# Kernel tuning notes

Measured on AMD Instinct MI355X. Metric: run time of the kernel, lower is better.

## Reference

```python
import jax, jax.numpy as jnp
import numpy as np

EPS = 1e-5  # eqx.nn.LayerNorm default


def _layer_norm(x, w, b):
    m = x.mean(-1, keepdims=True)
    v = ((x - m) ** 2).mean(-1, keepdims=True)
    return (x - m) / jnp.sqrt(v + EPS) * w + b


def _s4_block(x, nw, nb, lre, lim, bre, bim, cre, cim, d, lstep, ow, ob, o2w, o2b):
    # x: [L, H]. One SequenceBlock: LayerNorm -> S4 recurrence (lax.scan) -> GELU -> GLU-style gated linear -> residual.
    skip = x
    h = _layer_norm(x, nw, nb)
    Lam = lre + 1j * lim                      # [H, N] complex diagonal state matrix
    step = jnp.exp(lstep)[:, None]            # [H, 1] per-channel timescale
    BL = 1.0 / (1.0 - (step / 2.0) * Lam)     # bilinear discretization
    Abar = BL * (1.0 + (step / 2.0) * Lam)    # [H, N]
    Bbar = BL * step * (bre + 1j * bim)       # [H, N]
    C = cre + 1j * cim                        # [H, N]

    def scan_fn(state, u):                    # state: [H, N] complex, u: [H]
        new = Abar * state + Bbar * u[:, None]
        y = 2.0 * jnp.sum(C * new, axis=-1).real + d * u
        return new, y

    init = jnp.zeros(Abar.shape, Abar.dtype)  # cell.init_state
    _, y = jax.lax.scan(scan_fn, init, h)     # [L, H]
    y = jax.nn.gelu(y)
    y = (y @ ow.T + ob) * jax.nn.sigmoid(y @ o2w.T + o2b)
    return skip + y


def setup_inputs() -> dict:
    key = jax.random.key(0)
    L, IN, OUT, H, N, NL = 2048, 4, 3, 512, 32, 4
    ks = jax.random.split(key, 16)
    return {
        "x": jax.random.normal(ks[0], (L, IN), jnp.float32),
        "enc_w": jax.random.normal(ks[1], (H, IN), jnp.float32) / np.sqrt(IN),
        "enc_b": jnp.zeros((H,), jnp.float32),
        "dec_w": jax.random.normal(ks[2], (OUT, H), jnp.float32) / np.sqrt(H),
        "dec_b": jnp.zeros((OUT,), jnp.float32),
        "norm_w": jnp.ones((NL, H), jnp.float32),
        "norm_b": jnp.zeros((NL, H), jnp.float32),
        "lam_re": -0.5 - jax.random.uniform(ks[3], (NL, H, N), jnp.float32),  # stable (Re < 0)
        "lam_im": np.pi * jax.random.normal(ks[4], (NL, H, N), jnp.float32),
        "b_re": jax.random.normal(ks[5], (NL, H, N), jnp.float32) / np.sqrt(N),
        "b_im": jax.random.normal(ks[6], (NL, H, N), jnp.float32) / np.sqrt(N),
        "c_re": jax.random.normal(ks[7], (NL, H, N), jnp.float32) / np.sqrt(N),
        "c_im": jax.random.normal(ks[8], (NL, H, N), jnp.float32) / np.sqrt(N),
        "d": jax.random.normal(ks[9], (NL, H), jnp.float32),
        "log_step": float(np.log(1e-3)) + float(np.log(1e-1) - np.log(1e-3)) * jax.random.uniform(ks[10], (NL, H), jnp.float32),
        "out_w": jax.random.normal(ks[11], (NL, H, H), jnp.float32) / np.sqrt(H),
        "out_b": jnp.zeros((NL, H), jnp.float32),
        "out2_w": jax.random.normal(ks[12], (NL, H, H), jnp.float32) / np.sqrt(H),
        "out2_b": jnp.zeros((NL, H), jnp.float32),
    }


def reference(x, enc_w, enc_b, dec_w, dec_b, norm_w, norm_b, lam_re, lam_im, b_re, b_im, c_re, c_im, d, log_step, out_w, out_b, out2_w, out2_b):
    h = x @ enc_w.T + enc_b                   # encoder: [L, IN] -> [L, H]
    for i in range(norm_w.shape[0]):          # fixed small n_layers loop
        h = _s4_block(h, norm_w[i], norm_b[i], lam_re[i], lam_im[i], b_re[i], b_im[i],
                      c_re[i], c_im[i], d[i], log_step[i], out_w[i], out_b[i], out2_w[i], out2_b[i])
    return h @ dec_w.T + dec_b                # decoder: [L, H] -> [L, OUT]
```

## Files before the change

kernel.cpp:

```cpp
#include <hip/hip_runtime.h>
#include <hip/hip_bf16.h>
#include <math.h>

#define LSEQ 2048
#define HD   512
#define NST  32
#define LC   32
#define NCHK 64
#define SUP  8
#define NSUP 8
#define HH   (HD * HD)

typedef __bf16 bf16;
typedef __bf16 bf16x8 __attribute__((ext_vector_type(8)));
typedef float  floatx4 __attribute__((ext_vector_type(4)));

__device__ __forceinline__ float wave_reduce_add(float v) {
#pragma unroll
    for (int m = 32; m; m >>= 1) v += __shfl_xor(v, m, 64);
    return v;
}

__device__ __forceinline__ float gelu_tanh(float x) {
    float z = 0.7978845608028654f * (x + 0.044715f * x * x * x);
    float e = __expf(2.f * z);
    float th = 1.f - 2.f / (e + 1.f);
    return 0.5f * x * (1.f + th);
}

__device__ __forceinline__ void make_ab(float lre, float lim, float step,
                                        float br0, float bi0,
                                        float& ar, float& ai, float& br, float& bi) {
    float s2 = 0.5f * step;
    float dr = 1.f - s2 * lre, di = -s2 * lim;
    float inv = 1.f / (dr * dr + di * di);
    float blr = dr * inv, bli = -di * inv;
    float nr = 1.f + s2 * lre, ni = s2 * lim;
    ar = blr * nr - bli * ni;
    ai = blr * ni + bli * nr;
    float tr = step * br0, ti = step * bi0;
    br = blr * tr - bli * ti;
    bi = blr * ti + bli * tr;
}

__global__ __launch_bounds__(256) void prep_kernel(
    const float* __restrict__ lre, const float* __restrict__ lim,
    const float* __restrict__ bre, const float* __restrict__ bim,
    const float* __restrict__ cre, const float* __restrict__ cim,
    const float* __restrict__ ls,
    float2* __restrict__ cA, float2* __restrict__ cB,
    float2* __restrict__ cC, float2* __restrict__ cAp) {
    int tid = blockIdx.x * 256 + threadIdx.x;
    int lay = tid >> 14, rem = tid & 16383;
    int ch = rem >> 5, n = rem & 31;
    int src = tid;
    float step = __expf(ls[lay * HD + ch]);
    float ar, ai, br, bi;
    make_ab(lre[src], lim[src], step, bre[src], bim[src], ar, ai, br, bi);
    float xr = ar, xi = ai;
#pragma unroll
    for (int q = 0; q < 5; ++q) { float tt = xr * xr - xi * xi; xi = 2.f * xr * xi; xr = tt; }
    int dst = (lay * NST + n) * HD + ch;
    cA[dst]  = make_float2(ar, ai);
    cB[dst]  = make_float2(br, bi);
    cC[dst]  = make_float2(2.f * cre[src], 2.f * cim[src]);
    cAp[dst] = make_float2(xr, xi);
}

__global__ __launch_bounds__(256) void cvt_kernel(
    const float* __restrict__ ow, const float* __restrict__ o2w,
    bf16* __restrict__ wb) {
    const float* src = blockIdx.y ? o2w : ow;
    bf16* dst = wb + blockIdx.y * (4 * HH);
    int i = (blockIdx.x * 256 + threadIdx.x) * 8;
    float4 a = *(const float4*)(src + i);
    float4 b = *(const float4*)(src + i + 4);
    bf16x8 o;
    o[0] = (bf16)a.x; o[1] = (bf16)a.y; o[2] = (bf16)a.z; o[3] = (bf16)a.w;
    o[4] = (bf16)b.x; o[5] = (bf16)b.y; o[6] = (bf16)b.z; o[7] = (bf16)b.w;
    *(bf16x8*)(dst + i) = o;
}

__global__ __launch_bounds__(256) void enc_kernel(
    const float* __restrict__ x, const float* __restrict__ w,
    const float* __restrict__ b, float* __restrict__ h) {
    int idx = blockIdx.x * 256 + threadIdx.x;
    int t = idx >> 9, i = idx & (HD - 1);
    float acc = b[i];
    float4 xv = *(const float4*)(x + t * 4);
    float4 wv = *(const float4*)(w + i * 4);
    acc = fmaf(xv.x, wv.x, acc);
    acc = fmaf(xv.y, wv.y, acc);
    acc = fmaf(xv.z, wv.z, acc);
    acc = fmaf(xv.w, wv.w, acc);
    h[idx] = acc;
}

__global__ __launch_bounds__(256) void ln_kernel(
    const float* __restrict__ h, float* __restrict__ hn,
    const float* __restrict__ w, const float* __restrict__ b) {
    int wv = threadIdx.x >> 6, lane = threadIdx.x & 63;
    int row = blockIdx.x * 4 + wv;
    const float* hp = h + row * HD + lane * 8;
    float v[8];
    *(float4*)(v)     = *(const float4*)(hp);
    *(float4*)(v + 4) = *(const float4*)(hp + 4);
    float s = 0.f;
#pragma unroll
    for (int e = 0; e < 8; ++e) s += v[e];
    s = wave_reduce_add(s);
    float m = s * (1.f / HD);
    float q = 0.f;
#pragma unroll
    for (int e = 0; e < 8; ++e) { float d = v[e] - m; q += d * d; }
    q = wave_reduce_add(q);
    float rstd = rsqrtf(q * (1.f / HD) + 1e-5f);
    float w8[8], b8[8];
    *(float4*)(w8)     = *(const float4*)(w + lane * 8);
    *(float4*)(w8 + 4) = *(const float4*)(w + lane * 8 + 4);
    *(float4*)(b8)     = *(const float4*)(b + lane * 8);
    *(float4*)(b8 + 4) = *(const float4*)(b + lane * 8 + 4);
    float o[8];
#pragma unroll
    for (int e = 0; e < 8; ++e)
        o[e] = (v[e] - m) * rstd * w8[e] + b8[e];
    float* op = hn + row * HD + lane * 8;
    *(float4*)op       = *(float4*)o;
    *(float4*)(op + 4) = *(float4*)(o + 4);
}

__global__ __launch_bounds__(256, 2) void p1_kernel(
    const float* __restrict__ u,
    const float2* __restrict__ cA, const float2* __restrict__ cB,
    float2* __restrict__ f, int lay) {
    __shared__ float tile[4 * LC * 16];
    int tid = threadIdx.x;
    int lane = tid & 63, w = tid >> 6;
    int chl = lane & 15;
    int ch = blockIdx.x * 16 + chl;
    int sub = lane >> 4;
    int chunk = blockIdx.y * 4 + w;
    int t0 = blockIdx.y * 4 * LC;
    const float* ub = u + (size_t)t0 * HD + blockIdx.x * 16;
#pragma unroll
    for (int r = 0; r < 8; ++r) {
        int idx = r * 256 + tid;
        tile[idx] = ub[(idx >> 4) * HD + (idx & 15)];
    }
    int cbase = (lay * NST + sub * 8) * HD + ch;
    float aR[8], aI[8], bR[8], bI[8];
#pragma unroll
    for (int j = 0; j < 8; ++j) {
        float2 t = cA[cbase + j * HD]; aR[j] = t.x; aI[j] = t.y;
        t = cB[cbase + j * HD];        bR[j] = t.x; bI[j] = t.y;
    }
    float sr[8], si[8];
#pragma unroll
    for (int j = 0; j < 8; ++j) { sr[j] = 0.f; si[j] = 0.f; }
    __syncthreads();
    const float* tp = tile + (w * LC) * 16 + chl;
#pragma unroll 4
    for (int t = 0; t < LC; ++t) {
        float uu = tp[t * 16];
#pragma unroll
        for (int j = 0; j < 8; ++j) {
            float nr = fmaf(aR[j], sr[j], fmaf(-aI[j], si[j], bR[j] * uu));
            float ni = fmaf(aI[j], sr[j], fmaf( aR[j], si[j], bI[j] * uu));
            sr[j] = nr; si[j] = ni;
        }
    }
    float2* fp = f + (chunk * NST + sub * 8) * HD + ch;
#pragma unroll
    for (int j = 0; j < 8; ++j) fp[j * HD] = make_float2(sr[j], si[j]);
}

__global__ __launch_bounds__(256) void p2a_kernel(
    float2* __restrict__ f, const float2* __restrict__ cAp, int lay) {
    int tg = blockIdx.x * 256 + threadIdx.x;
    int ch = tg & 511;
    int ns = tg >> 9;
    int n = ns & 31, sup = ns >> 5;
    float2 ap = cAp[(lay * NST + n) * HD + ch];
    float2* fp = f + ((sup * SUP) * NST + n) * HD + ch;
    float sr = 0.f, si = 0.f;
#pragma unroll
    for (int j = 0; j < SUP; ++j) {
        float2 v = fp[(size_t)j * NST * HD];
        float nr = fmaf(ap.x, sr, fmaf(-ap.y, si, v.x));
        float ni = fmaf(ap.y, sr, fmaf( ap.x, si, v.y));
        sr = nr; si = ni;
        fp[(size_t)j * NST * HD] = make_float2(sr, si);
    }
}

__global__ __launch_bounds__(256) void p2b_kernel(
    float2* __restrict__ f, const float2* __restrict__ cAp, int lay) {
    int tg = blockIdx.x * 256 + threadIdx.x;
    int ch = tg & 511, n = tg >> 9;
    float2 ap = cAp[(lay * NST + n) * HD + ch];
    float xr = ap.x, xi = ap.y;
#pragma unroll
    for (int q = 0; q < 3; ++q) { float tt = xr * xr - xi * xi; xi = 2.f * xr * xi; xr = tt; }
    float2* fp = f + ((SUP - 1) * NST + n) * HD + ch;
    const size_t stride = (size_t)SUP * NST * HD;
    float sr = 0.f, si = 0.f;
#pragma unroll
    for (int k = 0; k < NSUP; ++k) {
        float2 v = fp[k * stride];
        float nr = fmaf(xr, sr, fmaf(-xi, si, v.x));
        float ni = fmaf(xi, sr, fmaf( xr, si, v.y));
        sr = nr; si = ni;
        fp[k * stride] = make_float2(sr, si);
    }
}

__global__ __launch_bounds__(256) void p2c_kernel(
    float2* __restrict__ f, const float2* __restrict__ cAp, int lay) {
    int tg = blockIdx.x * 256 + threadIdx.x;
    int ch = tg & 511;
    int ns = tg >> 9;
    int n = ns & 31, sup = ns >> 5;
    if (sup == 0) return;
    float2 ap = cAp[(lay * NST + n) * HD + ch];
    float2 S = f[((sup * SUP - 1) * NST + n) * HD + ch];
    float2* fp = f + ((sup * SUP) * NST + n) * HD + ch;
    float wr = ap.x, wi = ap.y;
#pragma unroll
    for (int j = 0; j < SUP - 1; ++j) {
        float2 v = fp[(size_t)j * NST * HD];
        v.x += wr * S.x - wi * S.y;
        v.y += wr * S.y + wi * S.x;
        fp[(size_t)j * NST * HD] = v;
        float nwr = wr * ap.x - wi * ap.y;
        float nwi = wr * ap.y + wi * ap.x;
        wr = nwr; wi = nwi;
    }
}

__global__ __launch_bounds__(256, 2) void p3_kernel(
    const float* __restrict__ u, const float2* __restrict__ f,
    const float2* __restrict__ cA, const float2* __restrict__ cB,
    const float2* __restrict__ cC, const float* __restrict__ d_p,
    bf16* __restrict__ g, int lay) {
    __shared__ float tile[4 * LC * 16];
    int tid = threadIdx.x;
    int lane = tid & 63, w = tid >> 6;
    int chl = lane & 15;
    int ch = blockIdx.x * 16 + chl;
    int sub = lane >> 4;
    int chunk = blockIdx.y * 4 + w;
    int t0 = blockIdx.y * 4 * LC;
    const float* ub = u + (size_t)t0 * HD + blockIdx.x * 16;
#pragma unroll
    for (int r = 0; r < 8; ++r) {
        int idx = r * 256 + tid;
        tile[idx] = ub[(idx >> 4) * HD + (idx & 15)];
    }
    int cbase = (lay * NST + sub * 8) * HD + ch;
    float aR[8], aI[8], bR[8], bI[8], cR[8], cI[8];
#pragma unroll
    for (int j = 0; j < 8; ++j) {
        float2 t = cA[cbase + j * HD]; aR[j] = t.x; aI[j] = t.y;
        t = cB[cbase + j * HD];        bR[j] = t.x; bI[j] = t.y;
        t = cC[cbase + j * HD];        cR[j] = t.x; cI[j] = t.y;
    }
    float dch = d_p[lay * HD + ch];
    float sr[8], si[8];
    if (chunk > 0) {
        const float2* ip = f + ((chunk - 1) * NST + sub * 8) * HD + ch;
#pragma unroll
        for (int j = 0; j < 8; ++j) { float2 v = ip[j * HD]; sr[j] = v.x; si[j] = v.y; }
    } else {
#pragma unroll
        for (int j = 0; j < 8; ++j) { sr[j] = 0.f; si[j] = 0.f; }
    }
    __syncthreads();
    const float* tp = tile + (w * LC) * 16 + chl;
    bf16* gp = g + (size_t)chunk * LC * HD + ch;
#pragma unroll 4
    for (int t = 0; t < LC; ++t) {
        float uu = tp[t * 16];
        float p = 0.f;
#pragma unroll
        for (int j = 0; j < 8; ++j) {
            float nr = fmaf(aR[j], sr[j], fmaf(-aI[j], si[j], bR[j] * uu));
            float ni = fmaf(aI[j], sr[j], fmaf( aR[j], si[j], bI[j] * uu));
            sr[j] = nr; si[j] = ni;
            p = fmaf(cR[j], nr, fmaf(-cI[j], ni, p));
        }
        p += __shfl_xor(p, 16);
        p += __shfl_xor(p, 32);
        float y = fmaf(dch, uu, p);
        if (sub == 0) gp[t * HD] = (bf16)gelu_tanh(y);
    }
}

__global__ __launch_bounds__(256) void mm_kernel(
    const bf16* __restrict__ A,
    const bf16* __restrict__ W1,
    const bf16* __restrict__ W2,
    const float* __restrict__ bias1, const float* __restrict__ bias2,
    float* __restrict__ Hio) {
    const int w = threadIdx.x >> 6, lane = threadIdx.x & 63;
    const int wm = w >> 1, wn = w & 1;
    const int mBase = blockIdx.y * 64 + wm * 32;
    const int nBase = blockIdx.x * 64 + wn * 32;
    const int lrow = lane & 15, quad = lane >> 4;

    floatx4 acc1[2][2] = {{{0.f,0.f,0.f,0.f},{0.f,0.f,0.f,0.f}},{{0.f,0.f,0.f,0.f},{0.f,0.f,0.f,0.f}}};
    floatx4 acc2[2][2] = {{{0.f,0.f,0.f,0.f},{0.f,0.f,0.f,0.f}},{{0.f,0.f,0.f,0.f},{0.f,0.f,0.f,0.f}}};

    for (int k0 = 0; k0 < HD; k0 += 32) {
        int kk = k0 + quad * 8;
        bf16x8 a0 = *(const bf16x8*)(A + (mBase + lrow) * HD + kk);
        bf16x8 a1 = *(const bf16x8*)(A + (mBase + 16 + lrow) * HD + kk);
        bf16x8 p0 = *(const bf16x8*)(W1 + (nBase + lrow) * HD + kk);
        bf16x8 p1 = *(const bf16x8*)(W1 + (nBase + 16 + lrow) * HD + kk);
        bf16x8 q0 = *(const bf16x8*)(W2 + (nBase + lrow) * HD + kk);
        bf16x8 q1 = *(const bf16x8*)(W2 + (nBase + 16 + lrow) * HD + kk);
        acc1[0][0] = __builtin_amdgcn_mfma_f32_16x16x32_bf16(a0, p0, acc1[0][0], 0, 0, 0);
        acc1[0][1] = __builtin_amdgcn_mfma_f32_16x16x32_bf16(a0, p1, acc1[0][1], 0, 0, 0);
        acc1[1][0] = __builtin_amdgcn_mfma_f32_16x16x32_bf16(a1, p0, acc1[1][0], 0, 0, 0);
        acc1[1][1] = __builtin_amdgcn_mfma_f32_16x16x32_bf16(a1, p1, acc1[1][1], 0, 0, 0);
        acc2[0][0] = __builtin_amdgcn_mfma_f32_16x16x32_bf16(a0, q0, acc2[0][0], 0, 0, 0);
        acc2[0][1] = __builtin_amdgcn_mfma_f32_16x16x32_bf16(a0, q1, acc2[0][1], 0, 0, 0);
        acc2[1][0] = __builtin_amdgcn_mfma_f32_16x16x32_bf16(a1, q0, acc2[1][0], 0, 0, 0);
        acc2[1][1] = __builtin_amdgcn_mfma_f32_16x16x32_bf16(a1, q1, acc2[1][1], 0, 0, 0);
    }

#pragma unroll
    for (int fm = 0; fm < 2; ++fm)
#pragma unroll
        for (int fn = 0; fn < 2; ++fn) {
            int j = nBase + fn * 16 + lrow;
            float bb1 = bias1[j], bb2 = bias2[j];
#pragma unroll
            for (int r = 0; r < 4; ++r) {
                int t = mBase + fm * 16 + quad * 4 + r;
                float z1 = acc1[fm][fn][r] + bb1;
                float z2 = acc2[fm][fn][r] + bb2;
                float val = z1 / (1.f + __expf(-z2));
                Hio[t * HD + j] += val;
            }
        }
}

__global__ __launch_bounds__(192) void dec_kernel(
    const float* __restrict__ h, const float* __restrict__ w,
    const float* __restrict__ b, float* __restrict__ out) {
    int j = threadIdx.x >> 6, lane = threadIdx.x & 63;
    int t = blockIdx.x;
    const float* hp = h + t * HD + lane * 8;
    float v[8];
    *(float4*)(v)     = *(const float4*)(hp);
    *(float4*)(v + 4) = *(const float4*)(hp + 4);
    float w8[8];
    *(float4*)(w8)     = *(const float4*)(w + j * HD + lane * 8);
    *(float4*)(w8 + 4) = *(const float4*)(w + j * HD + lane * 8 + 4);
    float s = 0.f;
#pragma unroll
    for (int e = 0; e < 8; ++e) s = fmaf(v[e], w8[e], s);
    s = wave_reduce_add(s);
    if (lane == 0) out[t * 3 + j] = s + b[j];
}

extern "C" void kernel_launch(void* const* d_in, const int* in_sizes, int n_in,
                              void* d_out, int out_size, void* d_ws, size_t ws_size,
                              hipStream_t stream) {
    const float* x   = (const float*)d_in[0];
    const float* ew  = (const float*)d_in[1];
    const float* eb  = (const float*)d_in[2];
    const float* dw  = (const float*)d_in[3];
    const float* db  = (const float*)d_in[4];
    const float* nw  = (const float*)d_in[5];
    const float* nb  = (const float*)d_in[6];
    const float* lre = (const float*)d_in[7];
    const float* lim = (const float*)d_in[8];
    const float* bre = (const float*)d_in[9];
    const float* bim = (const float*)d_in[10];
    const float* cre = (const float*)d_in[11];
    const float* cim = (const float*)d_in[12];
    const float* dd  = (const float*)d_in[13];
    const float* ls  = (const float*)d_in[14];
    const float* ow  = (const float*)d_in[15];
    const float* ob  = (const float*)d_in[16];
    const float* o2w = (const float*)d_in[17];
    const float* o2b = (const float*)d_in[18];

    char* ws = (char*)d_ws;
    float*  h   = (float*)ws;
    float*  hn  = (float*)(ws + (4  << 20));
    float2* f   = (float2*)(ws + (8  << 20));
    bf16*   g   = (bf16*)(ws + (24 << 20));
    bf16*   wb  = (bf16*)(ws + (26 << 20));
    float2* cA  = (float2*)(ws + (30 << 20));
    float2* cB  = (float2*)(ws + (30 << 20) + (512 << 10));
    float2* cC  = (float2*)(ws + (31 << 20));
    float2* cAp = (float2*)(ws + (31 << 20) + (512 << 10));

    prep_kernel<<<256, 256, 0, stream>>>(lre, lim, bre, bim, cre, cim, ls, cA, cB, cC, cAp);
    cvt_kernel<<<dim3(4 * HH / (256 * 8), 2), 256, 0, stream>>>(ow, o2w, wb);
    enc_kernel<<<LSEQ * HD / 256, 256, 0, stream>>>(x, ew, eb, h);
    for (int lay = 0; lay < 4; ++lay) {
        int oH = lay * HD;
        ln_kernel<<<LSEQ / 4, 256, 0, stream>>>(h, hn, nw + oH, nb + oH);
        p1_kernel<<<dim3(HD / 16, NCHK / 4), 256, 0, stream>>>(hn, cA, cB, f, lay);
        p2a_kernel<<<512, 256, 0, stream>>>(f, cAp, lay);
        p2b_kernel<<<64, 256, 0, stream>>>(f, cAp, lay);
        p2c_kernel<<<512, 256, 0, stream>>>(f, cAp, lay);
        p3_kernel<<<dim3(HD / 16, NCHK / 4), 256, 0, stream>>>(hn, f, cA, cB, cC, dd, g, lay);
        mm_kernel<<<dim3(HD / 64, LSEQ / 64), 256, 0, stream>>>(
            g, wb + lay * HH, wb + 4 * HH + lay * HH, ob + oH, o2b + oH, h);
    }
    dec_kernel<<<LSEQ, 192, 0, stream>>>(h, dw, db, (float*)d_out);
}
```

Before: 315.2 us.

## Fuse all stages into one persistent cooperative kernel with grid syncs

Replaces the 31-launch pipeline (prep, convert, encoder, per-layer LN, scan phases, GEMM, decoder) with a single cooperative kernel of 256 blocks that separates stages with grid.sync. LayerNorm is reduced to per-row stats and applied on the fly inside the scan phases, so the normalized activations are no longer written and read back. The intra-chunk scan reads activations through a shared-memory tile. A fallback keeps the old multi-kernel path if the cooperative launch fails. The aim is to remove launch overhead and inter-kernel gaps. The cost is that every phase is fixed at 256 blocks of 256 threads, which may lower occupancy for the GEMM and scan phases, and each grid sync adds latency.

```diff
diff --git a/kernel.cpp b/kernel.cpp
--- a/kernel.cpp
+++ b/kernel.cpp
@@ -1,6 +1,9 @@
 #include <hip/hip_runtime.h>
 #include <hip/hip_bf16.h>
+#include <hip/hip_cooperative_groups.h>
 #include <math.h>
+
+namespace cg = cooperative_groups;
 
 #define LSEQ 2048
 #define HD   512
@@ -10,6 +13,9 @@
 #define SUP  8
 #define NSUP 8
 #define HH   (HD * HD)
+#define GRID 256
+#define BLK  256
+#define NTH  (GRID * BLK)
 
 typedef __bf16 bf16;
 typedef __bf16 bf16x8 __attribute__((ext_vector_type(8)));
@@ -43,6 +49,315 @@
     bi = blr * ti + bli * tr;
 }
 
+__global__ __launch_bounds__(BLK, 1) void fused_kernel(
+    const float* __restrict__ x,   const float* __restrict__ ew,
+    const float* __restrict__ eb,  const float* __restrict__ dw,
+    const float* __restrict__ db,  const float* __restrict__ nw,
+    const float* __restrict__ nb,  const float* __restrict__ lre,
+    const float* __restrict__ lim, const float* __restrict__ bre,
+    const float* __restrict__ bim, const float* __restrict__ cre,
+    const float* __restrict__ cim, const float* __restrict__ dd,
+    const float* __restrict__ ls,  const float* __restrict__ ow,
+    const float* __restrict__ ob,  const float* __restrict__ o2w,
+    const float* __restrict__ o2b, float* __restrict__ out,
+    char* __restrict__ ws)
+{
+    cg::grid_group grid = cg::this_grid();
+
+    float*  h     = (float*)ws;
+    float2* f     = (float2*)(ws + (4  << 20));
+    float2* f2    = (float2*)(ws + (12 << 20));
+    bf16*   g     = (bf16*)(ws + (20 << 20));
+    bf16*   wb    = (bf16*)(ws + (22 << 20));
+    float2* stats = (float2*)(ws + (26 << 20));
+    float2* cA    = (float2*)(ws + (26 << 20) + (64 << 10));
+    float2* cB    = cA + 4 * NST * HD;
+    float2* cC    = cB + 4 * NST * HD;
+    float2* cAp   = cC + 4 * NST * HD;
+
+    const int bid = blockIdx.x, tid = threadIdx.x;
+    const int tg  = bid * BLK + tid;
+    const int lane = tid & 63, wv = tid >> 6;
+
+    __shared__ float  tile[4096];
+    __shared__ float2 sst[256];
+    __shared__ float  snw[16], snb[16];
+
+    {
+        int lay = tg >> 14, rem = tg & 16383;
+        int ch = rem >> 5, n = rem & 31;
+        float step = __expf(ls[lay * HD + ch]);
+        float ar, ai, br, bi;
+        make_ab(lre[tg], lim[tg], step, bre[tg], bim[tg], ar, ai, br, bi);
+        float xr = ar, xi = ai;
+#pragma unroll
+        for (int q = 0; q < 5; ++q) { float tt = xr * xr - xi * xi; xi = 2.f * xr * xi; xr = tt; }
+        int dst = (lay * NST + n) * HD + ch;
+        cA[dst]  = make_float2(ar, ai);
+        cB[dst]  = make_float2(br, bi);
+        cC[dst]  = make_float2(2.f * cre[tg], 2.f * cim[tg]);
+        cAp[dst] = make_float2(xr, xi);
+    }
+#pragma unroll
+    for (int it = 0; it < 2; ++it) {
+        int i = (it * NTH + tg) * 8;
+        float4 a = *(const float4*)(ow + i);
+        float4 b = *(const float4*)(ow + i + 4);
+        bf16x8 o;
+        o[0]=(bf16)a.x; o[1]=(bf16)a.y; o[2]=(bf16)a.z; o[3]=(bf16)a.w;
+        o[4]=(bf16)b.x; o[5]=(bf16)b.y; o[6]=(bf16)b.z; o[7]=(bf16)b.w;
+        *(bf16x8*)(wb + i) = o;
+        a = *(const float4*)(o2w + i);
+        b = *(const float4*)(o2w + i + 4);
+        o[0]=(bf16)a.x; o[1]=(bf16)a.y; o[2]=(bf16)a.z; o[3]=(bf16)a.w;
+        o[4]=(bf16)b.x; o[5]=(bf16)b.y; o[6]=(bf16)b.z; o[7]=(bf16)b.w;
+        *(bf16x8*)(wb + 4 * HH + i) = o;
+    }
+#pragma unroll
+    for (int it = 0; it < 16; ++it) {
+        int i = it * NTH + tg;
+        int t = i >> 9, c = i & 511;
+        float4 xv = *(const float4*)(x + t * 4);
+        float4 wv4 = *(const float4*)(ew + c * 4);
+        float acc = eb[c];
+        acc = fmaf(xv.x, wv4.x, acc); acc = fmaf(xv.y, wv4.y, acc);
+        acc = fmaf(xv.z, wv4.z, acc); acc = fmaf(xv.w, wv4.w, acc);
+        h[i] = acc;
+    }
+    grid.sync();
+
+    for (int lay = 0; lay < 4; ++lay) {
+#pragma unroll
+        for (int r = 0; r < 2; ++r) {
+            int row = bid * 8 + r * 4 + wv;
+            const float* hp = h + row * HD + lane * 8;
+            float v[8];
+            *(float4*)(v)     = *(const float4*)(hp);
+            *(float4*)(v + 4) = *(const float4*)(hp + 4);
+            float s = 0.f;
+#pragma unroll
+            for (int e = 0; e < 8; ++e) s += v[e];
+            s = wave_reduce_add(s);
+            float m = s * (1.f / HD);
+            float q = 0.f;
+#pragma unroll
+            for (int e = 0; e < 8; ++e) { float d = v[e] - m; q += d * d; }
+            q = wave_reduce_add(q);
+            float rstd = rsqrtf(q * (1.f / HD) + 1e-5f);
+            if (lane == 0) stats[row] = make_float2(m, rstd);
+        }
+        grid.sync();
+
+        const int bx = bid & 31, byy = bid >> 5;
+        const int t0 = byy * 256;
+        const int chl = lane & 15, ch = bx * 16 + chl, sub = lane >> 4;
+        const int cbase = (lay * NST + sub * 8) * HD + ch;
+
+        {
+            const float* ub = h + (size_t)t0 * HD + bx * 16;
+#pragma unroll
+            for (int rr = 0; rr < 16; ++rr) {
+                int idx = rr * 256 + tid;
+                tile[idx] = ub[(idx >> 4) * HD + (idx & 15)];
+            }
+            sst[tid] = stats[t0 + tid];
+            if (tid < 16) {
+                snw[tid] = nw[lay * HD + bx * 16 + tid];
+                snb[tid] = nb[lay * HD + bx * 16 + tid];
+            }
+            float aR[8], aI[8], bR[8], bI[8];
+#pragma unroll
+            for (int j = 0; j < 8; ++j) {
+                float2 t = cA[cbase + j * HD]; aR[j] = t.x; aI[j] = t.y;
+                t = cB[cbase + j * HD];        bR[j] = t.x; bI[j] = t.y;
+            }
+            __syncthreads();
+            float wch = snw[chl], bch = snb[chl];
+#pragma unroll
+            for (int k = 0; k < 2; ++k) {
+                int chunk = byy * 8 + wv * 2 + k;
+                float sr[8], si[8];
+#pragma unroll
+                for (int j = 0; j < 8; ++j) { sr[j] = 0.f; si[j] = 0.f; }
+#pragma unroll 4
+                for (int t = 0; t < LC; ++t) {
+                    int row = wv * 64 + k * 32 + t;
+                    float2 st = sst[row];
+                    float uu = (tile[row * 16 + chl] - st.x) * st.y * wch + bch;
+#pragma unroll
+                    for (int j = 0; j < 8; ++j) {
+                        float nr = fmaf(aR[j], sr[j], fmaf(-aI[j], si[j], bR[j] * uu));
+                        float ni = fmaf(aI[j], sr[j], fmaf( aR[j], si[j], bI[j] * uu));
+                        sr[j] = nr; si[j] = ni;
+                    }
+                }
+                float2* fp = f + ((size_t)chunk * NST + sub * 8) * HD + ch;
+#pragma unroll
+                for (int j = 0; j < 8; ++j) fp[j * HD] = make_float2(sr[j], si[j]);
+            }
+        }
+        grid.sync();
+
+#pragma unroll
+        for (int rep = 0; rep < 2; ++rep) {
+            int ii = rep * NTH + tg;
+            int cch = ii & 511, ns = ii >> 9;
+            int n = ns & 31, sup = ns >> 5;
+            float2 ap = cAp[(lay * NST + n) * HD + cch];
+            float2* fp = f + ((size_t)(sup * SUP) * NST + n) * HD + cch;
+            float sr = 0.f, si = 0.f;
+#pragma unroll
+            for (int j = 0; j < SUP; ++j) {
+                float2 v = fp[(size_t)j * NST * HD];
+                float nr = fmaf(ap.x, sr, fmaf(-ap.y, si, v.x));
+                float ni = fmaf(ap.y, sr, fmaf( ap.x, si, v.y));
+                sr = nr; si = ni;
+                fp[(size_t)j * NST * HD] = make_float2(sr, si);
+            }
+        }
+        grid.sync();
+
+#pragma unroll
+        for (int rep = 0; rep < 2; ++rep) {
+            int ii = rep * NTH + tg;
+            int cch = ii & 511, ns = ii >> 9;
+            int n = ns & 31, sup = ns >> 5;
+            float2 ap = cAp[(lay * NST + n) * HD + cch];
+            float a8r = ap.x, a8i = ap.y;
+#pragma unroll
+            for (int q = 0; q < 3; ++q) { float tt = a8r * a8r - a8i * a8i; a8i = 2.f * a8r * a8i; a8r = tt; }
+            float Sr = 0.f, Si = 0.f;
+            for (int k = 0; k < sup; ++k) {
+                float2 F = f[((size_t)(k * SUP + SUP - 1) * NST + n) * HD + cch];
+                float nr = fmaf(a8r, Sr, fmaf(-a8i, Si, F.x));
+                float ni = fmaf(a8i, Sr, fmaf( a8r, Si, F.y));
+                Sr = nr; Si = ni;
+            }
+            float wr = ap.x, wi = ap.y;
+            size_t base = ((size_t)(sup * SUP) * NST + n) * HD + cch;
+#pragma unroll
+            for (int j = 0; j < SUP; ++j) {
+                float2 v = f[base + (size_t)j * NST * HD];
+                v.x += wr * Sr - wi * Si;
+                v.y += wr * Si + wi * Sr;
+                f2[base + (size_t)j * NST * HD] = v;
+                float nwr = wr * ap.x - wi * ap.y;
+                float nwi = wr * ap.y + wi * ap.x;
+                wr = nwr; wi = nwi;
+            }
+        }
+        grid.sync();
+
+        {
+            float aR[8], aI[8], bR[8], bI[8], cR[8], cI[8];
+#pragma unroll
+            for (int j = 0; j < 8; ++j) {
+                float2 t = cA[cbase + j * HD]; aR[j] = t.x; aI[j] = t.y;
+                t = cB[cbase + j * HD];        bR[j] = t.x; bI[j] = t.y;
+                t = cC[cbase + j * HD];        cR[j] = t.x; cI[j] = t.y;
+            }
+            float dch = dd[lay * HD + ch];
+            float wch = snw[chl], bch = snb[chl];
+            int chunk0 = byy * 8 + wv * 2;
+            float sr[8], si[8];
+            if (chunk0 > 0) {
+                const float2* ip = f2 + ((size_t)(chunk0 - 1) * NST + sub * 8) * HD + ch;
+#pragma unroll
+                for (int j = 0; j < 8; ++j) { float2 v = ip[j * HD]; sr[j] = v.x; si[j] = v.y; }
+            } else {
+#pragma unroll
+                for (int j = 0; j < 8; ++j) { sr[j] = 0.f; si[j] = 0.f; }
+            }
+            bf16* gp = g + (size_t)t0 * HD + ch;
+#pragma unroll 4
+            for (int t = 0; t < 2 * LC; ++t) {
+                int row = wv * 64 + t;
+                float2 st = sst[row];
+                float uu = (tile[row * 16 + chl] - st.x) * st.y * wch + bch;
+                float p = 0.f;
+#pragma unroll
+                for (int j = 0; j < 8; ++j) {
+                    float nr = fmaf(aR[j], sr[j], fmaf(-aI[j], si[j], bR[j] * uu));
+                    float ni = fmaf(aI[j], sr[j], fmaf( aR[j], si[j], bI[j] * uu));
+                    sr[j] = nr; si[j] = ni;
+                    p = fmaf(cR[j], nr, fmaf(-cI[j], ni, p));
+                }
+                p += __shfl_xor(p, 16);
+                p += __shfl_xor(p, 32);
+                float y = fmaf(dch, uu, p);
+                if (sub == 0) gp[(size_t)row * HD] = (bf16)gelu_tanh(y);
+            }
+        }
+        grid.sync();
+
+        {
+            const bf16* W1 = wb + lay * HH;
+            const bf16* W2 = wb + 4 * HH + lay * HH;
+            const float* bias1 = ob + lay * HD;
+            const float* bias2 = o2b + lay * HD;
+            const int wm = wv >> 1, wn = wv & 1;
+            const int mBase = (bid >> 3) * 64 + wm * 32;
+            const int nBase = (bid & 7) * 64 + wn * 32;
+            const int lrow = lane & 15, quad = lane >> 4;
+            floatx4 acc1[2][2] = {{{0.f,0.f,0.f,0.f},{0.f,0.f,0.f,0.f}},{{0.f,0.f,0.f,0.f},{0.f,0.f,0.f,0.f}}};
+            floatx4 acc2[2][2] = {{{0.f,0.f,0.f,0.f},{0.f,0.f,0.f,0.f}},{{0.f,0.f,0.f,0.f},{0.f,0.f,0.f,0.f}}};
+            for (int k0 = 0; k0 < HD; k0 += 32) {
+                int kk = k0 + quad * 8;
+                bf16x8 a0 = *(const bf16x8*)(g + (mBase + lrow) * HD + kk);
+                bf16x8 a1 = *(const bf16x8*)(g + (mBase + 16 + lrow) * HD + kk);
+                bf16x8 p0 = *(const bf16x8*)(W1 + (nBase + lrow) * HD + kk);
+                bf16x8 p1 = *(const bf16x8*)(W1 + (nBase + 16 + lrow) * HD + kk);
+                bf16x8 q0 = *(const bf16x8*)(W2 + (nBase + lrow) * HD + kk);
+                bf16x8 q1 = *(const bf16x8*)(W2 + (nBase + 16 + lrow) * HD + kk);
+                acc1[0][0] = __builtin_amdgcn_mfma_f32_16x16x32_bf16(a0, p0, acc1[0][0], 0, 0, 0);
+                acc1[0][1] = __builtin_amdgcn_mfma_f32_16x16x32_bf16(a0, p1, acc1[0][1], 0, 0, 0);
+                acc1[1][0] = __builtin_amdgcn_mfma_f32_16x16x32_bf16(a1, p0, acc1[1][0], 0, 0, 0);
+                acc1[1][1] = __builtin_amdgcn_mfma_f32_16x16x32_bf16(a1, p1, acc1[1][1], 0, 0, 0);
+                acc2[0][0] = __builtin_amdgcn_mfma_f32_16x16x32_bf16(a0, q0, acc2[0][0], 0, 0, 0);
+                acc2[0][1] = __builtin_amdgcn_mfma_f32_16x16x32_bf16(a0, q1, acc2[0][1], 0, 0, 0);
+                acc2[1][0] = __builtin_amdgcn_mfma_f32_16x16x32_bf16(a1, q0, acc2[1][0], 0, 0, 0);
+                acc2[1][1] = __builtin_amdgcn_mfma_f32_16x16x32_bf16(a1, q1, acc2[1][1], 0, 0, 0);
+            }
+#pragma unroll
+            for (int fm = 0; fm < 2; ++fm)
+#pragma unroll
+                for (int fn = 0; fn < 2; ++fn) {
+                    int j = nBase + fn * 16 + lrow;
+                    float bb1 = bias1[j], bb2 = bias2[j];
+#pragma unroll
+                    for (int r = 0; r < 4; ++r) {
+                        int t = mBase + fm * 16 + quad * 4 + r;
+                        float z1 = acc1[fm][fn][r] + bb1;
+                        float z2 = acc2[fm][fn][r] + bb2;
+                        h[t * HD + j] += z1 / (1.f + __expf(-z2));
+                    }
+                }
+        }
+        grid.sync();
+    }
+
+#pragma unroll
+    for (int r = 0; r < 2; ++r) {
+        int row = bid * 8 + r * 4 + wv;
+        const float* hp = h + row * HD + lane * 8;
+        float v[8];
+        *(float4*)(v)     = *(const float4*)(hp);
+        *(float4*)(v + 4) = *(const float4*)(hp + 4);
+#pragma unroll
+        for (int j = 0; j < 3; ++j) {
+            const float* wp = dw + j * HD + lane * 8;
+            float w8[8];
+            *(float4*)(w8)     = *(const float4*)(wp);
+            *(float4*)(w8 + 4) = *(const float4*)(wp + 4);
+            float s = 0.f;
+#pragma unroll
+            for (int e = 0; e < 8; ++e) s = fmaf(v[e], w8[e], s);
+            s = wave_reduce_add(s);
+            if (lane == 0) out[row * 3 + j] = s + db[j];
+        }
+    }
+}
+
 __global__ __launch_bounds__(256) void prep_kernel(
     const float* __restrict__ lre, const float* __restrict__ lim,
     const float* __restrict__ bre, const float* __restrict__ bim,
@@ -53,17 +368,16 @@
     int tid = blockIdx.x * 256 + threadIdx.x;
     int lay = tid >> 14, rem = tid & 16383;
     int ch = rem >> 5, n = rem & 31;
-    int src = tid;
     float step = __expf(ls[lay * HD + ch]);
     float ar, ai, br, bi;
-    make_ab(lre[src], lim[src], step, bre[src], bim[src], ar, ai, br, bi);
+    make_ab(lre[tid], lim[tid], step, bre[tid], bim[tid], ar, ai, br, bi);
     float xr = ar, xi = ai;
 #pragma unroll
     for (int q = 0; q < 5; ++q) { float tt = xr * xr - xi * xi; xi = 2.f * xr * xi; xr = tt; }
     int dst = (lay * NST + n) * HD + ch;
     cA[dst]  = make_float2(ar, ai);
     cB[dst]  = make_float2(br, bi);
-    cC[dst]  = make_float2(2.f * cre[src], 2.f * cim[src]);
+    cC[dst]  = make_float2(2.f * cre[tid], 2.f * cim[tid]);
     cAp[dst] = make_float2(xr, xi);
 }
 
@@ -339,8 +653,7 @@
                 int t = mBase + fm * 16 + quad * 4 + r;
                 float z1 = acc1[fm][fn][r] + bb1;
                 float z2 = acc2[fm][fn][r] + bb2;
-                float val = z1 / (1.f + __expf(-z2));
-                Hio[t * HD + j] += val;
+                Hio[t * HD + j] += z1 / (1.f + __expf(-z2));
             }
         }
 }
@@ -386,31 +699,39 @@
     const float* ob  = (const float*)d_in[16];
     const float* o2w = (const float*)d_in[17];
     const float* o2b = (const float*)d_in[18];
-
-    char* ws = (char*)d_ws;
-    float*  h   = (float*)ws;
-    float*  hn  = (float*)(ws + (4  << 20));
-    float2* f   = (float2*)(ws + (8  << 20));
-    bf16*   g   = (bf16*)(ws + (24 << 20));
-    bf16*   wb  = (bf16*)(ws + (26 << 20));
-    float2* cA  = (float2*)(ws + (30 << 20));
-    float2* cB  = (float2*)(ws + (30 << 20) + (512 << 10));
-    float2* cC  = (float2*)(ws + (31 << 20));
-    float2* cAp = (float2*)(ws + (31 << 20) + (512 << 10));
-
-    prep_kernel<<<256, 256, 0, stream>>>(lre, lim, bre, bim, cre, cim, ls, cA, cB, cC, cAp);
-    cvt_kernel<<<dim3(4 * HH / (256 * 8), 2), 256, 0, stream>>>(ow, o2w, wb);
-    enc_kernel<<<LSEQ * HD / 256, 256, 0, stream>>>(x, ew, eb, h);
-    for (int lay = 0; lay < 4; ++lay) {
-        int oH = lay * HD;
-        ln_kernel<<<LSEQ / 4, 256, 0, stream>>>(h, hn, nw + oH, nb + oH);
-        p1_kernel<<<dim3(HD / 16, NCHK / 4), 256, 0, stream>>>(hn, cA, cB, f, lay);
-        p2a_kernel<<<512, 256, 0, stream>>>(f, cAp, lay);
-        p2b_kernel<<<64, 256, 0, stream>>>(f, cAp, lay);
-        p2c_kernel<<<512, 256, 0, stream>>>(f, cAp, lay);
-        p3_kernel<<<dim3(HD / 16, NCHK / 4), 256, 0, stream>>>(hn, f, cA, cB, cC, dd, g, lay);
-        mm_kernel<<<dim3(HD / 64, LSEQ / 64), 256, 0, stream>>>(
-            g, wb + lay * HH, wb + 4 * HH + lay * HH, ob + oH, o2b + oH, h);
-    }
-    dec_kernel<<<LSEQ, 192, 0, stream>>>(h, dw, db, (float*)d_out);
-}
+    float* outp = (float*)d_out;
+    char* wsp = (char*)d_ws;
+
+    void* args[] = { &x, &ew, &eb, &dw, &db, &nw, &nb, &lre, &lim, &bre, &bim,
+                     &cre, &cim, &dd, &ls, &ow, &ob, &o2w, &o2b, &outp, &wsp };
+    hipError_t err = hipLaunchCooperativeKernel((void*)fused_kernel, dim3(GRID),
+                                                dim3(BLK), args, 0, stream);
+    if (err != hipSuccess) {
+        (void)hipGetLastError();
+        float*  h   = (float*)wsp;
+        float*  hn  = (float*)(wsp + (4  << 20));
+        float2* f   = (float2*)(wsp + (8  << 20));
+        bf16*   g   = (bf16*)(wsp + (24 << 20));
+        bf16*   wb  = (bf16*)(wsp + (26 << 20));
+        float2* cA  = (float2*)(wsp + (30 << 20));
+        float2* cB  = (float2*)(wsp + (30 << 20) + (512 << 10));
+        float2* cC  = (float2*)(wsp + (31 << 20));
+        float2* cAp = (float2*)(wsp + (31 << 20) + (512 << 10));
+
+        prep_kernel<<<256, 256, 0, stream>>>(lre, lim, bre, bim, cre, cim, ls, cA, cB, cC, cAp);
+        cvt_kernel<<<dim3(4 * HH / (256 * 8), 2), 256, 0, stream>>>(ow, o2w, wb);
+        enc_kernel<<<LSEQ * HD / 256, 256, 0, stream>>>(x, ew, eb, h);
+        for (int lay = 0; lay < 4; ++lay) {
+            int oH = lay * HD;
+            ln_kernel<<<LSEQ / 4, 256, 0, stream>>>(h, hn, nw + oH, nb + oH);
+            p1_kernel<<<dim3(HD / 16, NCHK / 4), 256, 0, stream>>>(hn, cA, cB, f, lay);
+            p2a_kernel<<<512, 256, 0, stream>>>(f, cAp, lay);
+            p2b_kernel<<<64, 256, 0, stream>>>(f, cAp, lay);
+            p2c_kernel<<<512, 256, 0, stream>>>(f, cAp, lay);
+            p3_kernel<<<dim3(HD / 16, NCHK / 4), 256, 0, stream>>>(hn, f, cA, cB, cC, dd, g, lay);
+            mm_kernel<<<dim3(HD / 64, LSEQ / 64), 256, 0, stream>>>(
+                g, wb + lay * HH, wb + 4 * HH + lay * HH, ob + oH, o2b + oH, h);
+        }
+        dec_kernel<<<LSEQ, 192, 0, stream>>>(h, dw, db, outp);
+    }
+}
```

Result: slower. 1.101 ms (+249.5%).
